# Kernel optimization log

Measured on AMD Instinct MI355X. Metric: run time of the kernel, lower is better.

## Reference

```python
import jax, jax.numpy as jnp
import numpy as np

MAX_ITER = 20
F_TOL = 1e-6
FREE_NUM = 64  # free_idx[1] + 1
TRUNC = (0, 512)  # truncate_idx


def setup_inputs() -> dict:
    key = jax.random.key(0)
    ks = jax.random.split(key, 8)
    bsz, in_dim, hid, out_dim, m = 1024, 512, 1024, 256, 128
    return {
        "b_primal": jax.random.normal(ks[0], (bsz, in_dim), jnp.float32),
        "W0": jax.random.normal(ks[1], (hid, in_dim), jnp.float32) / np.sqrt(in_dim).astype(np.float32),
        "b0": jnp.zeros((hid,), jnp.float32),
        "W1": jax.random.normal(ks[2], (hid, hid), jnp.float32) / np.sqrt(hid).astype(np.float32),
        "b1": jnp.zeros((hid,), jnp.float32),
        "W2": jax.random.normal(ks[3], (out_dim, hid), jnp.float32) / np.sqrt(hid).astype(np.float32),
        "b2": jnp.zeros((out_dim,), jnp.float32),
        "A": jax.random.normal(ks[4], (m, out_dim), jnp.float32) * 0.1,
        "b_vec": jax.random.normal(ks[5], (m,), jnp.float32),
        # scaled so spectral norm < 1 -> contracting fixed-point iteration
        "WzProj": jax.random.normal(ks[6], (out_dim, out_dim), jnp.float32) * 0.03,
        "WbProj": jax.random.normal(ks[7], (out_dim, m), jnp.float32) * 0.1,
    }


def reference(b_primal, W0, b0, W1, b1, W2, b2, A, b_vec, WzProj, WbProj):
    # eval-mode forward of DualNN (report_projection=True)
    x = b_primal[:, TRUNC[0]:TRUNC[1]]
    h = jax.nn.relu(x @ W0.T + b0)
    h = jax.nn.relu(h @ W1.T + b1)
    out = h @ W2.T + b2                      # [bsz, output_dim]

    bias_proj = b_vec @ WbProj.T             # [output_dim]

    def cond(state):
        _, it, res = state
        return (it <= MAX_ITER) & (res > F_TOL)

    def body(state):
        z, it, _ = state
        z = bias_proj + z @ WzProj.T         # affine projection step
        u = z[:, :FREE_NUM]
        v = jax.nn.relu(z[:, FREE_NUM:])     # clamp non-free coordinates
        z = jnp.concatenate([u, v], axis=-1)
        res = jnp.max(jnp.abs(z @ A.T - b_vec))  # inf-norm equality residual
        return z, it + 1, res

    z_star, curr_iter, _ = jax.lax.while_loop(
        cond, body, (out, jnp.int32(1), jnp.float32(jnp.inf)))
    return (z_star, out, curr_iter)
```

## Files before the change

kernel.cpp:

```cpp
#include <hip/hip_runtime.h>

typedef __attribute__((ext_vector_type(8))) __bf16 bf16x8;
typedef __attribute__((ext_vector_type(4))) float f32x4;

#define MAX_ITER_N 20
#define F_TOL_F 1e-6f
#define FREE_NUM_N 64

#define BSZ 1024
#define IN_DIM 512
#define HID 1024
#define OUT_DIM 256
#define M_CON 128

#define WS_BAR   0
#define WS_RES   8
#define WS_BP    48
#define WS_H1    304
#define WS_H2    (WS_H1 + 524288)
#define WS_APC   (WS_H2 + 524288)
#define WS_W0C   (WS_APC + 262144)
#define WS_W1C   (WS_W0C + 262144)
#define WS_W2C   (WS_W1C + 524288)
#define WS_WZG   (WS_W2C + 131072)
#define WS_AG    (WS_WZG + 32768)

__device__ __forceinline__ unsigned short f2bf(float f) {
    unsigned int u = __float_as_uint(f);
    u += 0x7fffu + ((u >> 16) & 1u);
    return (unsigned short)(u >> 16);
}

__device__ __forceinline__ void gload_lds16(const unsigned short* g, unsigned short* l) {
    __builtin_amdgcn_global_load_lds(
        (const __attribute__((address_space(1))) unsigned int*)(const void*)g,
        (__attribute__((address_space(3))) unsigned int*)(void*)l, 16, 0, 0);
}

__global__ __launch_bounds__(256) void prep_k(
    const float* __restrict__ b_primal, const float* __restrict__ W0,
    const float* __restrict__ W1, const float* __restrict__ W2,
    const float* __restrict__ Wz, const float* __restrict__ Am,
    const float* __restrict__ b_vec, const float* __restrict__ WbProj,
    float* __restrict__ ws)
{
    unsigned short* APc = (unsigned short*)(ws + WS_APC);
    unsigned short* W0c = (unsigned short*)(ws + WS_W0C);
    unsigned short* W1c = (unsigned short*)(ws + WS_W1C);
    unsigned short* W2c = (unsigned short*)(ws + WS_W2C);
    unsigned short* WzG = (unsigned short*)(ws + WS_WZG);
    unsigned short* AG  = (unsigned short*)(ws + WS_AG);
    float* bp = ws + WS_BP;

    int b = blockIdx.x;
    int tid = threadIdx.x;
    if (b >= 2400) {
        float s = 0.0f;
        for (int k = 0; k < M_CON; ++k) s += b_vec[k] * WbProj[tid * M_CON + k];
        bp[tid] = s;
        return;
    }
    const float* src; unsigned short* dst; int off;
    if (b < 512)       { src = b_primal; dst = APc; off = b; }
    else if (b < 1024) { src = W0; dst = W0c; off = b - 512; }
    else if (b < 2048) { src = W1; dst = W1c; off = b - 1024; }
    else if (b < 2304) { src = W2; dst = W2c; off = b - 2048; }
    else if (b < 2368) { src = Wz; dst = WzG; off = b - 2304; }
    else               { src = Am; dst = AG;  off = b - 2368; }
    int idx = off * 1024 + tid * 4;
    float4 v = *(const float4*)(src + idx);
    ushort4 o;
    o.x = f2bf(v.x); o.y = f2bf(v.y); o.z = f2bf(v.z); o.w = f2bf(v.w);
    *(ushort4*)(dst + idx) = o;
}

__device__ __forceinline__ bf16x8 frag128(const unsigned short* lds, int row, int gc) {
    int phys = gc ^ (row & 15);
    return __builtin_bit_cast(bf16x8, *(const uint4*)(lds + row * 128 + phys * 8));
}

template<int K, int NTN, bool RELU, bool F32OUT>
__global__ __launch_bounds__(256, 4) void gemm32_k(
    const unsigned short* __restrict__ A,
    const unsigned short* __restrict__ B,
    const float* __restrict__ bias,
    void* __restrict__ Cv, int N_)
{
    constexpr int NCH = K / 128;
    __shared__ __align__(16) unsigned short As[2][32 * 128];
    __shared__ __align__(16) unsigned short Bs[2][32 * 128];

    const int tid = threadIdx.x;
    const int w = tid >> 6;
    const int lane = tid & 63;
    const int ln = lane & 15;
    const int q  = lane >> 4;
    const int wr = w >> 1;
    const int wc = w & 1;
    const int row0 = (blockIdx.x / NTN) * 32;
    const int col0 = (blockIdx.x % NTN) * 32;
    const unsigned short* Ab = A + row0 * K;
    const unsigned short* Bb = B + col0 * K;

    int soff[2], dbase[2];
#pragma unroll
    for (int i = 0; i < 2; ++i) {
        int P = w * 128 + i * 64 + lane;
        int row = P >> 4, pgc = P & 15;
        soff[i]  = row * K + (pgc ^ (row & 15)) * 8;
        dbase[i] = (w * 128 + i * 64) * 8;
    }

    f32x4 acc = {0.f, 0.f, 0.f, 0.f};

#pragma unroll
    for (int i = 0; i < 2; ++i) {
        gload_lds16(Ab + soff[i], &As[0][dbase[i]]);
        gload_lds16(Bb + soff[i], &Bs[0][dbase[i]]);
    }

    for (int c = 0; c < NCH; ++c) {
        __syncthreads();
        if (c + 1 < NCH) {
            const unsigned short* Ak = Ab + (c + 1) * 128;
            const unsigned short* Bk = Bb + (c + 1) * 128;
            int nb = (c + 1) & 1;
#pragma unroll
            for (int i = 0; i < 2; ++i) {
                gload_lds16(Ak + soff[i], &As[nb][dbase[i]]);
                gload_lds16(Bk + soff[i], &Bs[nb][dbase[i]]);
            }
        }
        const unsigned short* Ac = As[c & 1];
        const unsigned short* Bc = Bs[c & 1];
#pragma unroll
        for (int ks = 0; ks < 4; ++ks) {
            bf16x8 af = frag128(Ac, wr * 16 + ln, ks * 4 + q);
            bf16x8 bf = frag128(Bc, wc * 16 + ln, ks * 4 + q);
            acc = __builtin_amdgcn_mfma_f32_16x16x32_bf16(af, bf, acc, 0, 0, 0);
        }
    }

    const int c = col0 + wc * 16 + ln;
    const float bv = bias[c];
#pragma unroll
    for (int i = 0; i < 4; ++i) {
        int r = row0 + wr * 16 + q * 4 + i;
        float v = acc[i] + bv;
        if (RELU) v = fmaxf(v, 0.0f);
        if (F32OUT) ((float*)Cv)[r * N_ + c] = v;
        else ((unsigned short*)Cv)[r * N_ + c] = f2bf(v);
    }
}

__global__ __launch_bounds__(256, 1) void loop_k(
    const float* __restrict__ b_vec, float* __restrict__ out,
    float* __restrict__ ws)
{
    __shared__ __align__(16) unsigned char smem[16 * 264 * 2 + 256];
    unsigned int* res = (unsigned int*)(ws + WS_RES);
    float* bp = ws + WS_BP;
    const unsigned short* WzG = (const unsigned short*)(ws + WS_WZG);
    const unsigned short* AG  = (const unsigned short*)(ws + WS_AG);
    float* outz = out + BSZ * OUT_DIM;

    const int tid  = threadIdx.x;
    const int wave = tid >> 6;
    const int lane = tid & 63;
    const int ln   = lane & 15;
    const int q    = lane >> 4;
    const int r0   = blockIdx.x * 16;

    unsigned short (*zS)[264] = (unsigned short(*)[264])smem;
    float* red = (float*)(smem + 16 * 264 * 2);

    {
        int row = tid >> 4;
        int c0  = (tid & 15) * 16;
        const float* src = outz + (r0 + row) * OUT_DIM + c0;
#pragma unroll
        for (int i = 0; i < 16; ++i) zS[row][c0 + i] = f2bf(src[i]);
    }

    bf16x8 afr[2][8];
    float bvv[2];
#pragma unroll
    for (int mt = 0; mt < 2; ++mt) {
        int m = wave * 32 + mt * 16 + ln;
        bvv[mt] = b_vec[m];
#pragma unroll
        for (int ks = 0; ks < 8; ++ks)
            afr[mt][ks] = __builtin_bit_cast(bf16x8, *(const uint4*)(AG + m * OUT_DIM + ks * 32 + q * 8));
    }
    int colg[4];
    float bpv[4];
    bf16x8 wzfr[4][8];
#pragma unroll
    for (int nt = 0; nt < 4; ++nt) {
        colg[nt] = wave * 64 + nt * 16 + ln;
        bpv[nt]  = bp[colg[nt]];
#pragma unroll
        for (int ks = 0; ks < 8; ++ks)
            wzfr[nt][ks] = __builtin_bit_cast(bf16x8, *(const uint4*)(WzG + colg[nt] * OUT_DIM + ks * 32 + q * 8));
    }
    __syncthreads();

    bf16x8 zfr[8];
#pragma unroll
    for (int ks = 0; ks < 8; ++ks)
        zfr[ks] = __builtin_bit_cast(bf16x8, *(const uint4*)&zS[ln][ks * 32 + q * 8]);

    const f32x4 zero4 = {0.f, 0.f, 0.f, 0.f};

    for (int t = 1; t <= MAX_ITER_N; ++t) {
        f32x4 acc[4];
#pragma unroll
        for (int nt = 0; nt < 4; ++nt) acc[nt] = zero4;
#pragma unroll
        for (int ks = 0; ks < 8; ++ks)
#pragma unroll
            for (int nt = 0; nt < 4; ++nt)
                acc[nt] = __builtin_amdgcn_mfma_f32_16x16x32_bf16(zfr[ks], wzfr[nt][ks], acc[nt], 0, 0, 0);
        float vals[4][4];
#pragma unroll
        for (int nt = 0; nt < 4; ++nt)
#pragma unroll
            for (int i = 0; i < 4; ++i) {
                float v = acc[nt][i] + bpv[nt];
                if (colg[nt] >= FREE_NUM_N) v = fmaxf(v, 0.0f);
                vals[nt][i] = v;
            }
        if (t == MAX_ITER_N) {
#pragma unroll
            for (int nt = 0; nt < 4; ++nt)
#pragma unroll
                for (int i = 0; i < 4; ++i)
                    out[(r0 + q * 4 + i) * OUT_DIM + colg[nt]] = vals[nt][i];
        }
        __syncthreads();
#pragma unroll
        for (int nt = 0; nt < 4; ++nt)
#pragma unroll
            for (int i = 0; i < 4; ++i)
                zS[q * 4 + i][colg[nt]] = f2bf(vals[nt][i]);
        __syncthreads();
#pragma unroll
        for (int ks = 0; ks < 8; ++ks)
            zfr[ks] = __builtin_bit_cast(bf16x8, *(const uint4*)&zS[ln][ks * 32 + q * 8]);

        f32x4 acc2[2];
        acc2[0] = zero4; acc2[1] = zero4;
#pragma unroll
        for (int ks = 0; ks < 8; ++ks)
#pragma unroll
            for (int mt = 0; mt < 2; ++mt)
                acc2[mt] = __builtin_amdgcn_mfma_f32_16x16x32_bf16(zfr[ks], afr[mt][ks], acc2[mt], 0, 0, 0);
        float lmax = 0.0f;
#pragma unroll
        for (int mt = 0; mt < 2; ++mt)
#pragma unroll
            for (int i = 0; i < 4; ++i)
                lmax = fmaxf(lmax, fabsf(acc2[mt][i] - bvv[mt]));
#pragma unroll
        for (int off = 32; off > 0; off >>= 1)
            lmax = fmaxf(lmax, __shfl_xor(lmax, off));
        if (lane == 0) red[wave] = lmax;
        __syncthreads();
        if (tid == 0) {
            float bm = fmaxf(fmaxf(red[0], red[1]), fmaxf(red[2], red[3]));
            atomicMax(res + (t - 1), __float_as_uint(bm));
        }
    }
}

__global__ __launch_bounds__(256) void decide_fb_k(
    const float* __restrict__ WzProj, float* __restrict__ out,
    float* __restrict__ ws)
{
    __shared__ float zF[16][257];
    unsigned int* res = (unsigned int*)(ws + WS_RES);
    float* bp = ws + WS_BP;
    float* outz = out + BSZ * OUT_DIM;
    const int tid = threadIdx.x;

    int T = MAX_ITER_N;
    for (int t = 0; t < MAX_ITER_N; ++t) {
        float r = __uint_as_float(res[t]);
        if (!(r > F_TOL_F)) { T = t + 1; break; }
    }
    if (blockIdx.x == 0 && tid == 0)
        out[2 * BSZ * OUT_DIM] = (float)(T + 1);

    if (T >= MAX_ITER_N) return;

    const int r0 = blockIdx.x * 16;
    const int row = tid >> 4;
    const int c0 = (tid & 15) * 16;
    for (int i = 0; i < 16; ++i) zF[row][c0 + i] = outz[(r0 + row) * OUT_DIM + c0 + i];
    __syncthreads();
    const int j = tid;
    const float bj = bp[j];
    for (int t = 0; t < T; ++t) {
        float acc[16] = {};
        for (int k = 0; k < OUT_DIM; ++k) {
            float w = WzProj[j * OUT_DIM + k];
#pragma unroll
            for (int r = 0; r < 16; ++r) acc[r] += zF[r][k] * w;
        }
        __syncthreads();
#pragma unroll
        for (int r = 0; r < 16; ++r) {
            float v = acc[r] + bj;
            if (j >= FREE_NUM_N) v = fmaxf(v, 0.0f);
            zF[r][j] = v;
        }
        __syncthreads();
    }
    for (int i = 0; i < 16; ++i) out[(r0 + row) * OUT_DIM + c0 + i] = zF[row][c0 + i];
}

extern "C" void kernel_launch(void* const* d_in, const int* in_sizes, int n_in,
                              void* d_out, int out_size, void* d_ws, size_t ws_size,
                              hipStream_t stream) {
    const float* b_primal = (const float*)d_in[0];
    const float* W0     = (const float*)d_in[1];
    const float* b0     = (const float*)d_in[2];
    const float* W1     = (const float*)d_in[3];
    const float* b1     = (const float*)d_in[4];
    const float* W2     = (const float*)d_in[5];
    const float* b2     = (const float*)d_in[6];
    const float* Amat   = (const float*)d_in[7];
    const float* b_vec  = (const float*)d_in[8];
    const float* WzProj = (const float*)d_in[9];
    const float* WbProj = (const float*)d_in[10];
    float* out = (float*)d_out;
    float* ws  = (float*)d_ws;

    unsigned short* h1c = (unsigned short*)(ws + WS_H1);
    unsigned short* h2c = (unsigned short*)(ws + WS_H2);
    unsigned short* APc = (unsigned short*)(ws + WS_APC);
    unsigned short* W0c = (unsigned short*)(ws + WS_W0C);
    unsigned short* W1c = (unsigned short*)(ws + WS_W1C);
    unsigned short* W2c = (unsigned short*)(ws + WS_W2C);
    float* outz = out + BSZ * OUT_DIM;

    hipMemsetAsync(ws, 0, WS_BP * sizeof(float), stream);

    hipLaunchKernelGGL(prep_k, dim3(2401), dim3(256), 0, stream,
                       b_primal, W0, W1, W2, WzProj, Amat, b_vec, WbProj, ws);

    hipLaunchKernelGGL((gemm32_k<IN_DIM, 32, true, false>), dim3(1024), dim3(256), 0, stream,
                       APc, W0c, b0, (void*)h1c, HID);
    hipLaunchKernelGGL((gemm32_k<HID, 32, true, false>), dim3(1024), dim3(256), 0, stream,
                       h1c, W1c, b1, (void*)h2c, HID);
    hipLaunchKernelGGL((gemm32_k<HID, 8, false, true>), dim3(256), dim3(256), 0, stream,
                       h2c, W2c, b2, (void*)outz, OUT_DIM);

    hipLaunchKernelGGL(loop_k, dim3(64), dim3(256), 0, stream, b_vec, out, ws);
    hipLaunchKernelGGL(decide_fb_k, dim3(64), dim3(256), 0, stream, WzProj, out, ws);
}
```

Before: 140.2 us.

## Fuse fp32-to-bf16 conversion into GEMMs and merge pipeline into three kernels

```diff
diff --git a/kernel.cpp b/kernel.cpp
--- a/kernel.cpp
+++ b/kernel.cpp
@@ -18,10 +18,7 @@
 #define WS_BP    48
 #define WS_H1    304
 #define WS_H2    (WS_H1 + 524288)
-#define WS_APC   (WS_H2 + 524288)
-#define WS_W0C   (WS_APC + 262144)
-#define WS_W1C   (WS_W0C + 262144)
-#define WS_W2C   (WS_W1C + 524288)
+#define WS_W2C   (WS_H2 + 524288)
 #define WS_WZG   (WS_W2C + 131072)
 #define WS_AG    (WS_WZG + 32768)
 
@@ -31,47 +28,21 @@
     return (unsigned short)(u >> 16);
 }
 
+__device__ __forceinline__ uint4 cvt8(float4 a, float4 b) {
+    union { unsigned short s[8]; uint4 v; } u;
+    u.s[0] = f2bf(a.x); u.s[1] = f2bf(a.y); u.s[2] = f2bf(a.z); u.s[3] = f2bf(a.w);
+    u.s[4] = f2bf(b.x); u.s[5] = f2bf(b.y); u.s[6] = f2bf(b.z); u.s[7] = f2bf(b.w);
+    return u.v;
+}
+
 __device__ __forceinline__ void gload_lds16(const unsigned short* g, unsigned short* l) {
     __builtin_amdgcn_global_load_lds(
         (const __attribute__((address_space(1))) unsigned int*)(const void*)g,
         (__attribute__((address_space(3))) unsigned int*)(void*)l, 16, 0, 0);
 }
 
-__global__ __launch_bounds__(256) void prep_k(
-    const float* __restrict__ b_primal, const float* __restrict__ W0,
-    const float* __restrict__ W1, const float* __restrict__ W2,
-    const float* __restrict__ Wz, const float* __restrict__ Am,
-    const float* __restrict__ b_vec, const float* __restrict__ WbProj,
-    float* __restrict__ ws)
-{
-    unsigned short* APc = (unsigned short*)(ws + WS_APC);
-    unsigned short* W0c = (unsigned short*)(ws + WS_W0C);
-    unsigned short* W1c = (unsigned short*)(ws + WS_W1C);
-    unsigned short* W2c = (unsigned short*)(ws + WS_W2C);
-    unsigned short* WzG = (unsigned short*)(ws + WS_WZG);
-    unsigned short* AG  = (unsigned short*)(ws + WS_AG);
-    float* bp = ws + WS_BP;
-
-    int b = blockIdx.x;
-    int tid = threadIdx.x;
-    if (b >= 2400) {
-        float s = 0.0f;
-        for (int k = 0; k < M_CON; ++k) s += b_vec[k] * WbProj[tid * M_CON + k];
-        bp[tid] = s;
-        return;
-    }
-    const float* src; unsigned short* dst; int off;
-    if (b < 512)       { src = b_primal; dst = APc; off = b; }
-    else if (b < 1024) { src = W0; dst = W0c; off = b - 512; }
-    else if (b < 2048) { src = W1; dst = W1c; off = b - 1024; }
-    else if (b < 2304) { src = W2; dst = W2c; off = b - 2048; }
-    else if (b < 2368) { src = Wz; dst = WzG; off = b - 2304; }
-    else               { src = Am; dst = AG;  off = b - 2368; }
-    int idx = off * 1024 + tid * 4;
-    float4 v = *(const float4*)(src + idx);
-    ushort4 o;
-    o.x = f2bf(v.x); o.y = f2bf(v.y); o.z = f2bf(v.z); o.w = f2bf(v.w);
-    *(ushort4*)(dst + idx) = o;
+__device__ __forceinline__ bf16x8 ldfrag(const unsigned short* p) {
+    return __builtin_bit_cast(bf16x8, *(const uint4*)p);
 }
 
 __device__ __forceinline__ bf16x8 frag128(const unsigned short* lds, int row, int gc) {
@@ -79,17 +50,29 @@
     return __builtin_bit_cast(bf16x8, *(const uint4*)(lds + row * 128 + phys * 8));
 }
 
-template<int K, int NTN, bool RELU, bool F32OUT>
-__global__ __launch_bounds__(256, 4) void gemm32_k(
-    const unsigned short* __restrict__ A,
-    const unsigned short* __restrict__ B,
-    const float* __restrict__ bias,
-    void* __restrict__ Cv, int N_)
+__device__ __forceinline__ void grid_barrier(unsigned int* bar, unsigned int nblk) {
+    __syncthreads();
+    if (threadIdx.x == 0) {
+        unsigned int g = __hip_atomic_load(&bar[1], __ATOMIC_RELAXED, __HIP_MEMORY_SCOPE_AGENT);
+        unsigned int a = __hip_atomic_fetch_add(&bar[0], 1u, __ATOMIC_ACQ_REL, __HIP_MEMORY_SCOPE_AGENT);
+        if (a == nblk - 1u) {
+            __hip_atomic_store(&bar[0], 0u, __ATOMIC_RELAXED, __HIP_MEMORY_SCOPE_AGENT);
+            __hip_atomic_store(&bar[1], g + 1u, __ATOMIC_RELEASE, __HIP_MEMORY_SCOPE_AGENT);
+        } else {
+            while (__hip_atomic_load(&bar[1], __ATOMIC_ACQUIRE, __HIP_MEMORY_SCOPE_AGENT) == g)
+                __builtin_amdgcn_s_sleep(2);
+        }
+    }
+    __syncthreads();
+}
+
+template<int K, int NTN, bool AF32, bool BF32, bool RELU>
+__device__ __forceinline__ void gemm32_dev(
+    const void* __restrict__ Av, const void* __restrict__ Bv,
+    const float* __restrict__ bias, unsigned short* __restrict__ C, int N_,
+    int tile, unsigned short (*As)[32 * 128], unsigned short (*Bs)[32 * 128])
 {
     constexpr int NCH = K / 128;
-    __shared__ __align__(16) unsigned short As[2][32 * 128];
-    __shared__ __align__(16) unsigned short Bs[2][32 * 128];
-
     const int tid = threadIdx.x;
     const int w = tid >> 6;
     const int lane = tid & 63;
@@ -97,38 +80,81 @@
     const int q  = lane >> 4;
     const int wr = w >> 1;
     const int wc = w & 1;
-    const int row0 = (blockIdx.x / NTN) * 32;
-    const int col0 = (blockIdx.x % NTN) * 32;
-    const unsigned short* Ab = A + row0 * K;
-    const unsigned short* Bb = B + col0 * K;
-
-    int soff[2], dbase[2];
+    const int row0 = (tile / NTN) * 32;
+    const int col0 = (tile % NTN) * 32;
+
+    int goff[2], lgran[2], soff[2], dbase[2];
 #pragma unroll
     for (int i = 0; i < 2; ++i) {
-        int P = w * 128 + i * 64 + lane;
-        int row = P >> 4, pgc = P & 15;
-        soff[i]  = row * K + (pgc ^ (row & 15)) * 8;
-        dbase[i] = (w * 128 + i * 64) * 8;
+        int P = i * 256 + tid;
+        int row = P >> 4, gc = P & 15;
+        goff[i]  = row * K + gc * 8;
+        lgran[i] = row * 128 + (gc ^ (row & 15)) * 8;
+        int base = w * 128 + i * 64;
+        int P2 = base + lane;
+        int row2 = P2 >> 4, pgc = P2 & 15;
+        soff[i]  = row2 * K + (pgc ^ (row2 & 15)) * 8;
+        dbase[i] = base * 8;
+    }
+
+    const float* Af = (const float*)Av + row0 * K;
+    const float* Bf = (const float*)Bv + col0 * K;
+    const unsigned short* Ah = (const unsigned short*)Av + row0 * K;
+    const unsigned short* Bh = (const unsigned short*)Bv + col0 * K;
+
+    float4 fa[2][2], fb[2][2];
+    if constexpr (AF32) {
+#pragma unroll
+        for (int i = 0; i < 2; ++i) {
+            fa[i][0] = *(const float4*)(Af + goff[i]);
+            fa[i][1] = *(const float4*)(Af + goff[i] + 4);
+        }
+#pragma unroll
+        for (int i = 0; i < 2; ++i) *(uint4*)&As[0][lgran[i]] = cvt8(fa[i][0], fa[i][1]);
+    } else {
+#pragma unroll
+        for (int i = 0; i < 2; ++i) gload_lds16(Ah + soff[i], &As[0][dbase[i]]);
+    }
+    if constexpr (BF32) {
+#pragma unroll
+        for (int i = 0; i < 2; ++i) {
+            fb[i][0] = *(const float4*)(Bf + goff[i]);
+            fb[i][1] = *(const float4*)(Bf + goff[i] + 4);
+        }
+#pragma unroll
+        for (int i = 0; i < 2; ++i) *(uint4*)&Bs[0][lgran[i]] = cvt8(fb[i][0], fb[i][1]);
+    } else {
+#pragma unroll
+        for (int i = 0; i < 2; ++i) gload_lds16(Bh + soff[i], &Bs[0][dbase[i]]);
     }
 
     f32x4 acc = {0.f, 0.f, 0.f, 0.f};
 
-#pragma unroll
-    for (int i = 0; i < 2; ++i) {
-        gload_lds16(Ab + soff[i], &As[0][dbase[i]]);
-        gload_lds16(Bb + soff[i], &Bs[0][dbase[i]]);
-    }
-
     for (int c = 0; c < NCH; ++c) {
         __syncthreads();
+        const int nb = (c + 1) & 1;
         if (c + 1 < NCH) {
-            const unsigned short* Ak = Ab + (c + 1) * 128;
-            const unsigned short* Bk = Bb + (c + 1) * 128;
-            int nb = (c + 1) & 1;
-#pragma unroll
-            for (int i = 0; i < 2; ++i) {
-                gload_lds16(Ak + soff[i], &As[nb][dbase[i]]);
-                gload_lds16(Bk + soff[i], &Bs[nb][dbase[i]]);
+            if constexpr (AF32) {
+#pragma unroll
+                for (int i = 0; i < 2; ++i) {
+                    fa[i][0] = *(const float4*)(Af + (c + 1) * 128 + goff[i]);
+                    fa[i][1] = *(const float4*)(Af + (c + 1) * 128 + goff[i] + 4);
+                }
+            } else {
+#pragma unroll
+                for (int i = 0; i < 2; ++i)
+                    gload_lds16(Ah + (c + 1) * 128 + soff[i], &As[nb][dbase[i]]);
+            }
+            if constexpr (BF32) {
+#pragma unroll
+                for (int i = 0; i < 2; ++i) {
+                    fb[i][0] = *(const float4*)(Bf + (c + 1) * 128 + goff[i]);
+                    fb[i][1] = *(const float4*)(Bf + (c + 1) * 128 + goff[i] + 4);
+                }
+            } else {
+#pragma unroll
+                for (int i = 0; i < 2; ++i)
+                    gload_lds16(Bh + (c + 1) * 128 + soff[i], &Bs[nb][dbase[i]]);
             }
         }
         const unsigned short* Ac = As[c & 1];
@@ -139,27 +165,88 @@
             bf16x8 bf = frag128(Bc, wc * 16 + ln, ks * 4 + q);
             acc = __builtin_amdgcn_mfma_f32_16x16x32_bf16(af, bf, acc, 0, 0, 0);
         }
-    }
-
-    const int c = col0 + wc * 16 + ln;
-    const float bv = bias[c];
+        if (c + 1 < NCH) {
+            if constexpr (AF32) {
+#pragma unroll
+                for (int i = 0; i < 2; ++i) *(uint4*)&As[nb][lgran[i]] = cvt8(fa[i][0], fa[i][1]);
+            }
+            if constexpr (BF32) {
+#pragma unroll
+                for (int i = 0; i < 2; ++i) *(uint4*)&Bs[nb][lgran[i]] = cvt8(fb[i][0], fb[i][1]);
+            }
+        }
+    }
+
+    const int cc = col0 + wc * 16 + ln;
+    const float bv = bias[cc];
 #pragma unroll
     for (int i = 0; i < 4; ++i) {
         int r = row0 + wr * 16 + q * 4 + i;
         float v = acc[i] + bv;
         if (RELU) v = fmaxf(v, 0.0f);
-        if (F32OUT) ((float*)Cv)[r * N_ + c] = v;
-        else ((unsigned short*)Cv)[r * N_ + c] = f2bf(v);
-    }
+        C[r * N_ + cc] = f2bf(v);
+    }
+}
+
+__global__ __launch_bounds__(256, 4) void g1_k(
+    const float* __restrict__ b_primal, const float* __restrict__ W0,
+    const float* __restrict__ b0, float* __restrict__ ws)
+{
+    __shared__ __align__(16) unsigned short As[2][32 * 128];
+    __shared__ __align__(16) unsigned short Bs[2][32 * 128];
+    if (blockIdx.x == 0 && threadIdx.x < 40)
+        ((unsigned int*)ws)[threadIdx.x] = 0u;
+    unsigned short* h1c = (unsigned short*)(ws + WS_H1);
+    gemm32_dev<IN_DIM, 32, true, true, true>(b_primal, W0, b0, h1c, HID,
+                                             blockIdx.x, As, Bs);
+}
+
+__global__ __launch_bounds__(256, 4) void g2_k(
+    const float* __restrict__ W1, const float* __restrict__ b1,
+    const float* __restrict__ W2, const float* __restrict__ Wz,
+    const float* __restrict__ Amat, const float* __restrict__ b_vec,
+    const float* __restrict__ WbProj, float* __restrict__ ws)
+{
+    __shared__ __align__(16) unsigned short As[2][32 * 128];
+    __shared__ __align__(16) unsigned short Bs[2][32 * 128];
+    const int tid = threadIdx.x;
+    if (blockIdx.x >= 1024) {
+        int b = blockIdx.x - 1024;
+        if (b == 352) {
+            float s = 0.0f;
+            const float* wrow = WbProj + tid * M_CON;
+            for (int k = 0; k < M_CON; ++k) s += b_vec[k] * wrow[k];
+            (ws + WS_BP)[tid] = s;
+            return;
+        }
+        const float* src; unsigned short* dst; int off;
+        if (b < 256)      { src = W2;   dst = (unsigned short*)(ws + WS_W2C); off = b; }
+        else if (b < 320) { src = Wz;   dst = (unsigned short*)(ws + WS_WZG); off = b - 256; }
+        else              { src = Amat; dst = (unsigned short*)(ws + WS_AG);  off = b - 320; }
+        int idx = off * 1024 + tid * 4;
+        float4 v = *(const float4*)(src + idx);
+        ushort4 o;
+        o.x = f2bf(v.x); o.y = f2bf(v.y); o.z = f2bf(v.z); o.w = f2bf(v.w);
+        *(ushort4*)(dst + idx) = o;
+        return;
+    }
+    const unsigned short* h1c = (const unsigned short*)(ws + WS_H1);
+    unsigned short* h2c = (unsigned short*)(ws + WS_H2);
+    gemm32_dev<HID, 32, false, true, true>(h1c, W1, b1, h2c, HID,
+                                           blockIdx.x, As, Bs);
 }
 
 __global__ __launch_bounds__(256, 1) void loop_k(
-    const float* __restrict__ b_vec, float* __restrict__ out,
+    const float* __restrict__ b2, const float* __restrict__ b_vec,
+    const float* __restrict__ WzProj, float* __restrict__ out,
     float* __restrict__ ws)
 {
-    __shared__ __align__(16) unsigned char smem[16 * 264 * 2 + 256];
+    __shared__ __align__(16) unsigned char smem[16 * 257 * 4 + 64];
+    unsigned int* bar = (unsigned int*)(ws + WS_BAR);
     unsigned int* res = (unsigned int*)(ws + WS_RES);
-    float* bp = ws + WS_BP;
+    const float* bp = ws + WS_BP;
+    const unsigned short* h2c = (const unsigned short*)(ws + WS_H2);
+    const unsigned short* W2c = (const unsigned short*)(ws + WS_W2C);
     const unsigned short* WzG = (const unsigned short*)(ws + WS_WZG);
     const unsigned short* AG  = (const unsigned short*)(ws + WS_AG);
     float* outz = out + BSZ * OUT_DIM;
@@ -172,15 +259,39 @@
     const int r0   = blockIdx.x * 16;
 
     unsigned short (*zS)[264] = (unsigned short(*)[264])smem;
-    float* red = (float*)(smem + 16 * 264 * 2);
+    float* red = (float*)(smem + 16 * 257 * 4);
+
+    int colg[4];
+#pragma unroll
+    for (int nt = 0; nt < 4; ++nt) colg[nt] = wave * 64 + nt * 16 + ln;
 
     {
-        int row = tid >> 4;
-        int c0  = (tid & 15) * 16;
-        const float* src = outz + (r0 + row) * OUT_DIM + c0;
-#pragma unroll
-        for (int i = 0; i < 16; ++i) zS[row][c0 + i] = f2bf(src[i]);
-    }
+        f32x4 acc0[4];
+#pragma unroll
+        for (int nt = 0; nt < 4; ++nt) acc0[nt] = (f32x4){0.f, 0.f, 0.f, 0.f};
+        const unsigned short* arow = h2c + (r0 + ln) * HID + q * 8;
+#pragma unroll 2
+        for (int kf = 0; kf < 32; ++kf) {
+            bf16x8 af = ldfrag(arow + kf * 32);
+#pragma unroll
+            for (int nt = 0; nt < 4; ++nt) {
+                bf16x8 bf = ldfrag(W2c + colg[nt] * HID + kf * 32 + q * 8);
+                acc0[nt] = __builtin_amdgcn_mfma_f32_16x16x32_bf16(af, bf, acc0[nt], 0, 0, 0);
+            }
+        }
+        float b2v[4];
+#pragma unroll
+        for (int nt = 0; nt < 4; ++nt) b2v[nt] = b2[colg[nt]];
+#pragma unroll
+        for (int nt = 0; nt < 4; ++nt)
+#pragma unroll
+            for (int i = 0; i < 4; ++i) {
+                float v = acc0[nt][i] + b2v[nt];
+                outz[(r0 + q * 4 + i) * OUT_DIM + colg[nt]] = v;
+                zS[q * 4 + i][colg[nt]] = f2bf(v);
+            }
+    }
+    __builtin_amdgcn_sched_barrier(0);
 
     bf16x8 afr[2][8];
     float bvv[2];
@@ -190,18 +301,16 @@
         bvv[mt] = b_vec[m];
 #pragma unroll
         for (int ks = 0; ks < 8; ++ks)
-            afr[mt][ks] = __builtin_bit_cast(bf16x8, *(const uint4*)(AG + m * OUT_DIM + ks * 32 + q * 8));
-    }
-    int colg[4];
+            afr[mt][ks] = ldfrag(AG + m * OUT_DIM + ks * 32 + q * 8);
+    }
     float bpv[4];
     bf16x8 wzfr[4][8];
 #pragma unroll
     for (int nt = 0; nt < 4; ++nt) {
-        colg[nt] = wave * 64 + nt * 16 + ln;
-        bpv[nt]  = bp[colg[nt]];
+        bpv[nt] = bp[colg[nt]];
 #pragma unroll
         for (int ks = 0; ks < 8; ++ks)
-            wzfr[nt][ks] = __builtin_bit_cast(bf16x8, *(const uint4*)(WzG + colg[nt] * OUT_DIM + ks * 32 + q * 8));
+            wzfr[nt][ks] = ldfrag(WzG + colg[nt] * OUT_DIM + ks * 32 + q * 8);
     }
     __syncthreads();
 
@@ -271,17 +380,8 @@
             atomicMax(res + (t - 1), __float_as_uint(bm));
         }
     }
-}
-
-__global__ __launch_bounds__(256) void decide_fb_k(
-    const float* __restrict__ WzProj, float* __restrict__ out,
-    float* __restrict__ ws)
-{
-    __shared__ float zF[16][257];
-    unsigned int* res = (unsigned int*)(ws + WS_RES);
-    float* bp = ws + WS_BP;
-    float* outz = out + BSZ * OUT_DIM;
-    const int tid = threadIdx.x;
+
+    grid_barrier(bar, 64);
 
     int T = MAX_ITER_N;
     for (int t = 0; t < MAX_ITER_N; ++t) {
@@ -291,32 +391,33 @@
     if (blockIdx.x == 0 && tid == 0)
         out[2 * BSZ * OUT_DIM] = (float)(T + 1);
 
-    if (T >= MAX_ITER_N) return;
-
-    const int r0 = blockIdx.x * 16;
-    const int row = tid >> 4;
-    const int c0 = (tid & 15) * 16;
-    for (int i = 0; i < 16; ++i) zF[row][c0 + i] = outz[(r0 + row) * OUT_DIM + c0 + i];
-    __syncthreads();
-    const int j = tid;
-    const float bj = bp[j];
-    for (int t = 0; t < T; ++t) {
-        float acc[16] = {};
-        for (int k = 0; k < OUT_DIM; ++k) {
-            float w = WzProj[j * OUT_DIM + k];
-#pragma unroll
-            for (int r = 0; r < 16; ++r) acc[r] += zF[r][k] * w;
-        }
-        __syncthreads();
-#pragma unroll
-        for (int r = 0; r < 16; ++r) {
-            float v = acc[r] + bj;
-            if (j >= FREE_NUM_N) v = fmaxf(v, 0.0f);
-            zF[r][j] = v;
-        }
-        __syncthreads();
-    }
-    for (int i = 0; i < 16; ++i) out[(r0 + row) * OUT_DIM + c0 + i] = zF[row][c0 + i];
+    if (T < MAX_ITER_N) {
+        float (*zF)[257] = (float(*)[257])smem;
+        const int row = tid >> 4;
+        const int c0 = (tid & 15) * 16;
+        __syncthreads();
+        for (int i = 0; i < 16; ++i) zF[row][c0 + i] = outz[(r0 + row) * OUT_DIM + c0 + i];
+        __syncthreads();
+        const int j = tid;
+        const float bj = bp[j];
+        for (int t = 0; t < T; ++t) {
+            float acc[16] = {};
+            for (int k = 0; k < OUT_DIM; ++k) {
+                float w = WzProj[j * OUT_DIM + k];
+#pragma unroll
+                for (int r = 0; r < 16; ++r) acc[r] += zF[r][k] * w;
+            }
+            __syncthreads();
+#pragma unroll
+            for (int r = 0; r < 16; ++r) {
+                float v = acc[r] + bj;
+                if (j >= FREE_NUM_N) v = fmaxf(v, 0.0f);
+                zF[r][j] = v;
+            }
+            __syncthreads();
+        }
+        for (int i = 0; i < 16; ++i) out[(r0 + row) * OUT_DIM + c0 + i] = zF[row][c0 + i];
+    }
 }
 
 extern "C" void kernel_launch(void* const* d_in, const int* in_sizes, int n_in,
@@ -336,26 +437,10 @@
     float* out = (float*)d_out;
     float* ws  = (float*)d_ws;
 
-    unsigned short* h1c = (unsigned short*)(ws + WS_H1);
-    unsigned short* h2c = (unsigned short*)(ws + WS_H2);
-    unsigned short* APc = (unsigned short*)(ws + WS_APC);
-    unsigned short* W0c = (unsigned short*)(ws + WS_W0C);
-    unsigned short* W1c = (unsigned short*)(ws + WS_W1C);
-    unsigned short* W2c = (unsigned short*)(ws + WS_W2C);
-    float* outz = out + BSZ * OUT_DIM;
-
-    hipMemsetAsync(ws, 0, WS_BP * sizeof(float), stream);
-
-    hipLaunchKernelGGL(prep_k, dim3(2401), dim3(256), 0, stream,
-                       b_primal, W0, W1, W2, WzProj, Amat, b_vec, WbProj, ws);
-
-    hipLaunchKernelGGL((gemm32_k<IN_DIM, 32, true, false>), dim3(1024), dim3(256), 0, stream,
-                       APc, W0c, b0, (void*)h1c, HID);
-    hipLaunchKernelGGL((gemm32_k<HID, 32, true, false>), dim3(1024), dim3(256), 0, stream,
-                       h1c, W1c, b1, (void*)h2c, HID);
-    hipLaunchKernelGGL((gemm32_k<HID, 8, false, true>), dim3(256), dim3(256), 0, stream,
-                       h2c, W2c, b2, (void*)outz, OUT_DIM);
-
-    hipLaunchKernelGGL(loop_k, dim3(64), dim3(256), 0, stream, b_vec, out, ws);
-    hipLaunchKernelGGL(decide_fb_k, dim3(64), dim3(256), 0, stream, WzProj, out, ws);
-}
+    hipLaunchKernelGGL(g1_k, dim3(1024), dim3(256), 0, stream,
+                       b_primal, W0, b0, ws);
+    hipLaunchKernelGGL(g2_k, dim3(1024 + 353), dim3(256), 0, stream,
+                       W1, b1, W2, WzProj, Amat, b_vec, WbProj, ws);
+    hipLaunchKernelGGL(loop_k, dim3(64), dim3(256), 0, stream,
+                       b2, b_vec, WzProj, out, ws);
+}
```

After: 152.4 us. +8.8%, slower.
